# Performance work log

Measured on AMD Instinct MI355X. Metric: run time of the kernel, lower is better.

Reference implementation:

```python
import jax, jax.numpy as jnp
import numpy as np

B, H, W, C, N, P = 4, 200, 176, 256, 16384, 65536
EPS = 1e-3  # BatchNorm eps from the torch module


def _bn(x, g, b, axes):
    # training-mode batch norm (batch statistics), matching nn.BatchNorm forward
    m = x.mean(axes, keepdims=True)
    v = x.var(axes, keepdims=True)
    return (x - m) * jax.lax.rsqrt(v + EPS) * g + b


def setup_inputs() -> dict:
    key = jax.random.key(0)
    ks = jax.random.split(key, 16)
    s = 0.05
    d = {}
    d['feats'] = jax.random.normal(ks[0], (B, C, N), jnp.float32)
    d['cb'] = jax.random.randint(ks[1], (P,), 0, B, dtype=jnp.int32)
    d['cy'] = jax.random.randint(ks[2], (P,), 0, H, dtype=jnp.int32)
    d['cx'] = jax.random.randint(ks[3], (P,), 0, W, dtype=jnp.int32)
    # SH head: Linear(256,256,nb)+BN+ReLU, Linear(256,256,nb)+BN+ReLU, Linear(256,9,b)
    d['sh_w1'] = jax.random.normal(ks[4], (C, 256), jnp.float32) * s
    d['sh_g1'] = jnp.ones((256,), jnp.float32); d['sh_b1'] = jnp.zeros((256,), jnp.float32)
    d['sh_w2'] = jax.random.normal(ks[5], (256, 256), jnp.float32) * s
    d['sh_g2'] = jnp.ones((256,), jnp.float32); d['sh_b2'] = jnp.zeros((256,), jnp.float32)
    d['sh_w3'] = jax.random.normal(ks[6], (256, 9), jnp.float32) * s
    d['sh_bias3'] = jnp.zeros((9,), jnp.float32)
    # Gaus head: Linear(256,256,nb)+BN+ReLU, Linear(256,128,nb)+BN+ReLU, Linear(128,1,b)+sigmoid
    d['g_w1'] = jax.random.normal(ks[7], (C, 256), jnp.float32) * s
    d['g_g1'] = jnp.ones((256,), jnp.float32); d['g_b1'] = jnp.zeros((256,), jnp.float32)
    d['g_w2'] = jax.random.normal(ks[8], (256, 128), jnp.float32) * s
    d['g_g2'] = jnp.ones((128,), jnp.float32); d['g_b2'] = jnp.zeros((128,), jnp.float32)
    d['g_w3'] = jax.random.normal(ks[9], (128, 1), jnp.float32) * s
    d['g_bias3'] = jnp.zeros((1,), jnp.float32)
    # conv_out: 3x3 SparseConv2d no-bias + BN + ReLU ; shared_conv: 3x3 SubMConv2d bias + BN + ReLU
    d['cw1'] = jax.random.normal(ks[10], (3, 3, C, C), jnp.float32) * s
    d['c1_g'] = jnp.ones((C,), jnp.float32); d['c1_b'] = jnp.zeros((C,), jnp.float32)
    d['cw2'] = jax.random.normal(ks[11], (3, 3, C, C), jnp.float32) * s
    d['c2_bias'] = jnp.zeros((C,), jnp.float32)
    d['c2_g'] = jnp.ones((C,), jnp.float32); d['c2_b'] = jnp.zeros((C,), jnp.float32)
    return d


def reference(feats, cb, cy, cx, sh_w1, sh_g1, sh_b1, sh_w2, sh_g2, sh_b2, sh_w3, sh_bias3,
              g_w1, g_g1, g_b1, g_w2, g_g2, g_b2, g_w3, g_bias3,
              cw1, c1_g, c1_b, cw2, c2_bias, c2_g, c2_b):
    # [B,C,N] -> [B*N, C] point-wise features
    pw = feats.transpose(0, 2, 1).reshape(-1, C)
    # pool_feature_in_same_voxel: mean of point features sharing a voxel
    vid = cb * (H * W) + cy * W + cx  # [P] linear voxel id over dense BEV grid
    S = B * H * W
    sums = jax.ops.segment_sum(pw, vid, num_segments=S)            # [S, C]
    cnt = jax.ops.segment_sum(jnp.ones((P,), pw.dtype), vid, num_segments=S)
    pooled = sums / jnp.maximum(cnt, 1.0)[:, None]                 # [S, C]
    # SH head
    h = jax.nn.relu(_bn(pooled @ sh_w1, sh_g1, sh_b1, 0))
    h = jax.nn.relu(_bn(h @ sh_w2, sh_g2, sh_b2, 0))
    pred_sh = h @ sh_w3 + sh_bias3                                 # [S, 9]
    # Gaussian head
    g = jax.nn.relu(_bn(pooled @ g_w1, g_g1, g_b1, 0))
    g = jax.nn.relu(_bn(g @ g_w2, g_g2, g_b2, 0))
    pred_gaus = jax.nn.sigmoid(g @ g_w3 + g_bias3)                 # [S, 1]
    # get_sparse_voxel_feature3: SH (DC term) + gaussian modulated voxel features
    sp = pooled * pred_gaus * pred_sh[:, :1]                       # [S, C]
    x = sp.reshape(B, H, W, C)                                      # dense BEV sparse-tensor equivalent
    dn = ('NHWC', 'HWIO', 'NHWC')
    x = jax.lax.conv_general_dilated(x, cw1, (1, 1), 'SAME', dimension_numbers=dn)
    x = jax.nn.relu(_bn(x, c1_g, c1_b, (0, 1, 2)))
    x = jax.lax.conv_general_dilated(x, cw2, (1, 1), 'SAME', dimension_numbers=dn) + c2_bias
    x = jax.nn.relu(_bn(x, c2_g, c2_b, (0, 1, 2)))
    return x
```

## Files before the change

kernel.cpp:

```cpp
#include <hip/hip_runtime.h>
#include <hip/hip_bf16.h>
#include <cstdint>
#include <cstddef>

#define B_DIM 4
#define H_DIM 200
#define W_DIM 176
#define CCH 256
#define NPP 16384
#define NPTS 65536
#define HW 35200
#define S_TOT 140800
#define EPS 1e-3f
#define INV_S (1.0f/140800.0f)

typedef unsigned short ushort_t;
typedef __attribute__((ext_vector_type(8))) short bf16x8;
typedef __attribute__((ext_vector_type(4))) float f32x4;

__device__ __forceinline__ ushort_t f2bf(float f) {
    __hip_bfloat16 h = __float2bfloat16(f);
    return *(ushort_t*)&h;
}
__device__ __forceinline__ float bf2f(ushort_t u) {
    __hip_bfloat16 h = *(__hip_bfloat16*)&u;
    return __bfloat162float(h);
}

__device__ __forceinline__ void async16(const void* g, void* l) {
    __builtin_amdgcn_global_load_lds(
        (const __attribute__((address_space(1))) unsigned int*)g,
        (__attribute__((address_space(3))) unsigned int*)l,
        16, 0, 0);
}

__device__ __forceinline__ int xcd_virt(int fid, int n) {
    int q = n >> 3, r = n & 7;
    int xcd = fid & 7, idx = fid >> 3;
    int base = (xcd < r) ? xcd * (q + 1) : r * (q + 1) + (xcd - r) * q;
    return base + idx;
}

__global__ __launch_bounds__(256) void k_transpose(
    const float* __restrict__ feats, float* __restrict__ FT)
{
    __shared__ float lds[64][65];
    const int b  = blockIdx.z;
    const int c0 = blockIdx.y * 64;
    const int n0 = blockIdx.x * 64;
    const int tid = threadIdx.x;
#pragma unroll
    for (int i = 0; i < 16; ++i) {
        int idx = i * 256 + tid;
        int cr = idx >> 6, nc = idx & 63;
        lds[cr][nc] = feats[((size_t)b * 256 + c0 + cr) * NPP + n0 + nc];
    }
    __syncthreads();
#pragma unroll
    for (int i = 0; i < 16; ++i) {
        int idx = i * 256 + tid;
        int nr = idx >> 6, cc = idx & 63;
        FT[((size_t)b * NPP + n0 + nr) * CCH + c0 + cc] = lds[cc][nr];
    }
}

__global__ __launch_bounds__(256) void k_buildidx(
    const int* __restrict__ cb, const int* __restrict__ cy,
    const int* __restrict__ cx, int* __restrict__ cnt,
    int* __restrict__ pslot, int* __restrict__ vid)
{
    int p = blockIdx.x * 256 + threadIdx.x;
    int v = cb[p] * HW + cy[p] * W_DIM + cx[p];
    vid[p] = v;
    int r = atomicAdd(&cnt[v], 1);
    if (r < 8) pslot[v * 8 + r] = p;
}

__global__ __launch_bounds__(256) void k_poolgather(
    const float* __restrict__ FT, const int* __restrict__ cnt,
    const int* __restrict__ pslot, const int* __restrict__ vid,
    ushort_t* __restrict__ Pb)
{
    const int wave = threadIdx.x >> 6;
    const int lane = threadIdx.x & 63;
    const int v = blockIdx.x * 4 + wave;
    const int c = cnt[v];
    float4 a = make_float4(0.f, 0.f, 0.f, 0.f);
    if (c <= 8) {
        for (int k = 0; k < c; ++k) {
            int p = pslot[v * 8 + k];
            float4 r = ((const float4*)(FT + (size_t)p * CCH))[lane];
            a.x += r.x; a.y += r.y; a.z += r.z; a.w += r.w;
        }
    } else {
        for (int p = 0; p < NPTS; ++p)
            if (vid[p] == v) {
                float4 r = ((const float4*)(FT + (size_t)p * CCH))[lane];
                a.x += r.x; a.y += r.y; a.z += r.z; a.w += r.w;
            }
    }
    float inv = c ? 1.f / (float)c : 0.f;
    ushort4 o;
    o.x = f2bf(a.x * inv); o.y = f2bf(a.y * inv);
    o.z = f2bf(a.z * inv); o.w = f2bf(a.w * inv);
    ((ushort4*)(Pb + (size_t)v * CCH))[lane] = o;
}

__global__ __launch_bounds__(256) void k_gemmma(
    const ushort_t* __restrict__ X, const ushort_t* __restrict__ Wt,
    ushort_t* __restrict__ Y1, ushort_t* __restrict__ Y2, int ldY,
    int bnh, int nblocks,
    float* __restrict__ acc0, float* __restrict__ acc1, int sqoff)
{
    __shared__ ushort_t Asm[128 * 64];
    __shared__ ushort_t Bsm[128 * 64];
    const int tid  = threadIdx.x;
    const int w    = tid >> 6;
    const int lane = tid & 63;
    const int virt = xcd_virt(blockIdx.x, nblocks);
    const int pi   = virt / bnh;
    const int bn   = (virt % bnh) * 128;
    const int bm   = pi * 128;
    const int wr   = (w >> 1) * 64;
    const int wc   = (w & 1) * 64;

    size_t aoff[4]; size_t boff[4];
#pragma unroll
    for (int j = 0; j < 4; ++j) {
        int row  = 32 * j + 8 * w + (lane >> 3);
        int qlog = (lane & 7) ^ (row & 7);
        aoff[j] = (size_t)(bm + row) * 256 + qlog * 8;
        boff[j] = (size_t)(bn + row) * 256 + qlog * 8;
    }

    f32x4 acc[4][4] = {};
    for (int kc = 0; kc < 256; kc += 64) {
#pragma unroll
        for (int j = 0; j < 4; ++j)
            async16(X + aoff[j] + kc, Asm + (j * 32 + w * 8) * 64);
#pragma unroll
        for (int j = 0; j < 4; ++j)
            async16(Wt + boff[j] + kc, Bsm + (j * 32 + w * 8) * 64);
        __syncthreads();
#pragma unroll
        for (int ks = 0; ks < 2; ++ks) {
            const int q = ks * 4 + (lane >> 4);
            bf16x8 af[4], bfr[4];
#pragma unroll
            for (int i = 0; i < 4; ++i) {
                int ra = wr + i * 16 + (lane & 15);
                af[i] = *(const bf16x8*)&Asm[ra * 64 + ((q ^ (ra & 7)) * 8)];
            }
#pragma unroll
            for (int jn = 0; jn < 4; ++jn) {
                int rn = wc + jn * 16 + (lane & 15);
                bfr[jn] = *(const bf16x8*)&Bsm[rn * 64 + ((q ^ (rn & 7)) * 8)];
            }
#pragma unroll
            for (int i = 0; i < 4; ++i)
#pragma unroll
                for (int jn = 0; jn < 4; ++jn)
                    acc[i][jn] = __builtin_amdgcn_mfma_f32_16x16x32_bf16(
                        af[i], bfr[jn], acc[i][jn], 0, 0, 0);
        }
        __syncthreads();
    }

    const int crow0 = bm + wr + (lane >> 4) * 4;
    const int ccol0 = bn + wc + (lane & 15);
    float ls[4] = {}, lq[4] = {};
#pragma unroll
    for (int i = 0; i < 4; ++i)
#pragma unroll
        for (int jn = 0; jn < 4; ++jn) {
            int col = ccol0 + jn * 16;
#pragma unroll
            for (int r = 0; r < 4; ++r) {
                float v = acc[i][jn][r];
                ls[jn] += v; lq[jn] += v * v;
                size_t row = (size_t)(crow0 + i * 16 + r);
                if (col < 256) Y1[row * ldY + col] = f2bf(v);
                else           Y2[row * ldY + col - 256] = f2bf(v);
            }
        }
#pragma unroll
    for (int jn = 0; jn < 4; ++jn) {
        ls[jn] += __shfl_xor(ls[jn], 16, 64); ls[jn] += __shfl_xor(ls[jn], 32, 64);
        lq[jn] += __shfl_xor(lq[jn], 16, 64); lq[jn] += __shfl_xor(lq[jn], 32, 64);
    }
    float* red = (float*)Asm;
    if (lane < 16) {
#pragma unroll
        for (int jn = 0; jn < 4; ++jn) {
            red[((w * 16 + lane) * 4 + jn) * 2 + 0] = ls[jn];
            red[((w * 16 + lane) * 4 + jn) * 2 + 1] = lq[jn];
        }
    }
    __syncthreads();
    if (tid < 256) {
        int colhalf = tid & 127, isq = tid >> 7;
        int pair = colhalf >> 6, within = colhalf & 63;
        int l16 = within & 15, jn = within >> 4;
        int w0 = pair ? 1 : 0, w1 = pair ? 3 : 2;
        float s = red[((w0 * 16 + l16) * 4 + jn) * 2 + isq]
                + red[((w1 * 16 + l16) * 4 + jn) * 2 + isq];
        int colg = bn + colhalf;
        float* t = (colg < 256) ? acc0 : acc1;
        atomicAdd(&t[(colg & 255) + isq * sqoff], s);
    }
}

__global__ __launch_bounds__(256) void k_convmma(
    const ushort_t* __restrict__ X, const ushort_t* __restrict__ Wt,
    float* __restrict__ Yf, ushort_t* __restrict__ Yb,
    const float* __restrict__ bias, const ushort_t* __restrict__ zp,
    float* __restrict__ accp)
{
    __shared__ ushort_t Asm[2][192 * 64];
    __shared__ ushort_t Bsm[2][128 * 64];
    const int tid  = threadIdx.x;
    const int w    = tid >> 6;
    const int lane = tid & 63;
    const int virt = xcd_virt(blockIdx.x, 2200);
    const int pi   = virt >> 1;
    const int bn   = (virt & 1) * 128;
    const int b    = pi / 275;
    const int rem  = pi % 275;
    const int th   = rem / 11, tw = rem % 11;
    const int y0   = th * 8 - 1, x0 = tw * 16 - 1;
    const int hb   = (w >> 1) * 4;
    const int wc   = (w & 1) * 64;

    const int qlog = (lane & 7) ^ (lane >> 3);
    const ushort_t* asrc[6];
#pragma unroll
    for (int j = 0; j < 6; ++j) {
        int hr = j * 32 + w * 8 + (lane >> 3);
        int ph = hr / 18, pw = hr % 18;
        int y = y0 + ph, x = x0 + pw;
        bool ok = (hr < 180) && ((unsigned)y < (unsigned)H_DIM) &&
                  ((unsigned)x < (unsigned)W_DIM);
        asrc[j] = ok ? X + ((size_t)b * HW + (size_t)y * W_DIM + x) * 256 + qlog * 8
                     : zp + (lane & 7) * 8;
    }
    const ushort_t* bsrc = Wt + (size_t)(bn + w * 8 + (lane >> 3)) * 256 + qlog * 8;
    const int ldsoff = (w * 8) * 64;

#pragma unroll
    for (int j = 0; j < 6; ++j)
        async16(asrc[j], &Asm[0][(j * 32) * 64 + ldsoff]);
#pragma unroll
    for (int j = 0; j < 4; ++j)
        async16(bsrc + (size_t)j * 8192, &Bsm[0][(j * 32) * 64 + ldsoff]);
    __syncthreads();

    f32x4 acc[4][4] = {};
    for (int kc = 0; kc < 4; ++kc) {
        const ushort_t* acur = Asm[kc & 1];
#pragma unroll
        for (int pos = 0; pos < 9; ++pos) {
            const ushort_t* bcur = Bsm[(kc + pos) & 1];
            ushort_t* bnxt = (ushort_t*)Bsm[(kc + pos + 1) & 1];
            if (pos < 8) {
#pragma unroll
                for (int j = 0; j < 4; ++j)
                    async16(bsrc + (size_t)(pos + 1) * 65536 + kc * 64 + j * 8192,
                            bnxt + (j * 32) * 64 + ldsoff);
            } else if (kc < 3) {
#pragma unroll
                for (int j = 0; j < 4; ++j)
                    async16(bsrc + (size_t)(kc + 1) * 64 + j * 8192,
                            bnxt + (j * 32) * 64 + ldsoff);
#pragma unroll
                for (int j = 0; j < 6; ++j)
                    async16(asrc[j] + (kc + 1) * 64,
                            &Asm[(kc + 1) & 1][(j * 32) * 64 + ldsoff]);
            }
            const int dy = pos / 3 - 1, dx = pos % 3 - 1;
#pragma unroll
            for (int ks = 0; ks < 2; ++ks) {
                const int q = ks * 4 + (lane >> 4);
                bf16x8 af[4], bfr[4];
#pragma unroll
                for (int i = 0; i < 4; ++i) {
                    int ri = (hb + i + 1 + dy) * 18 + 1 + dx + (lane & 15);
                    af[i] = *(const bf16x8*)&acur[ri * 64 + ((q ^ (ri & 7)) * 8)];
                }
#pragma unroll
                for (int jn = 0; jn < 4; ++jn) {
                    int rn = wc + jn * 16 + (lane & 15);
                    bfr[jn] = *(const bf16x8*)&bcur[rn * 64 + ((q ^ (rn & 7)) * 8)];
                }
#pragma unroll
                for (int i = 0; i < 4; ++i)
#pragma unroll
                    for (int jn = 0; jn < 4; ++jn)
                        acc[i][jn] = __builtin_amdgcn_mfma_f32_16x16x32_bf16(
                            af[i], bfr[jn], acc[i][jn], 0, 0, 0);
            }
            __syncthreads();
        }
    }

    const size_t sbase = (size_t)b * HW + (size_t)(th * 8) * W_DIM + tw * 16;
    const int colb = bn + wc + (lane & 15);
    const int wsub = (lane >> 4) * 4;
    float ls[4] = {}, lq[4] = {};
#pragma unroll
    for (int i = 0; i < 4; ++i) {
        int h = hb + i;
#pragma unroll
        for (int jn = 0; jn < 4; ++jn) {
            int col = colb + jn * 16;
            float bb = bias ? bias[col] : 0.f;
#pragma unroll
            for (int r = 0; r < 4; ++r) {
                size_t s = sbase + (size_t)h * W_DIM + wsub + r;
                float v = acc[i][jn][r] + bb;
                ls[jn] += v; lq[jn] += v * v;
                size_t o = s * 256 + col;
                if (Yb) Yb[o] = f2bf(v); else Yf[o] = v;
            }
        }
    }
#pragma unroll
    for (int jn = 0; jn < 4; ++jn) {
        ls[jn] += __shfl_xor(ls[jn], 16, 64); ls[jn] += __shfl_xor(ls[jn], 32, 64);
        lq[jn] += __shfl_xor(lq[jn], 16, 64); lq[jn] += __shfl_xor(lq[jn], 32, 64);
    }
    float* red = (float*)&Asm[0][0];
    if (lane < 16) {
#pragma unroll
        for (int jn = 0; jn < 4; ++jn) {
            red[((w * 16 + lane) * 4 + jn) * 2 + 0] = ls[jn];
            red[((w * 16 + lane) * 4 + jn) * 2 + 1] = lq[jn];
        }
    }
    __syncthreads();
    if (tid < 256) {
        int colhalf = tid & 127, isq = tid >> 7;
        int pair = colhalf >> 6, within = colhalf & 63;
        int l16 = within & 15, jn = within >> 4;
        int w0 = pair ? 1 : 0, w1 = pair ? 3 : 2;
        float s = red[((w0 * 16 + l16) * 4 + jn) * 2 + isq]
                + red[((w1 * 16 + l16) * 4 + jn) * 2 + isq];
        atomicAdd(&accp[(bn + colhalf) + isq * 256], s);
    }
}

__global__ __launch_bounds__(256) void k_castw(
    const float* __restrict__ Wc, ushort_t* __restrict__ Wt, int CO)
{
    int pc = blockIdx.x;
    int co = pc % CO, pos = pc / CO, ci = threadIdx.x;
    Wt[(size_t)pc * 256 + ci] = f2bf(Wc[((size_t)pos * 256 + ci) * CO + co]);
}

__global__ void k_bnparams(const float* __restrict__ acc,
                           const float* __restrict__ g,
                           const float* __restrict__ b,
                           float* __restrict__ par, int ncols)
{
    int c = threadIdx.x;
    if (c >= ncols) return;
    float m = acc[c] * INV_S;
    float v = acc[ncols + c] * INV_S - m * m;
    float sc = g[c] * rsqrtf(v + EPS);
    par[c] = sc;
    par[ncols + c] = b[c] - m * sc;
}

__global__ __launch_bounds__(256) void k_bnrelu_bf(
    ushort_t* __restrict__ Y, const float* __restrict__ par)
{
    size_t q = (size_t)blockIdx.x * 256 + threadIdx.x;
    int c = (int)(q & 63) * 4;
    ushort4 u = ((ushort4*)Y)[q];
    u.x = f2bf(fmaxf(0.f, bf2f(u.x) * par[c + 0] + par[256 + c + 0]));
    u.y = f2bf(fmaxf(0.f, bf2f(u.y) * par[c + 1] + par[256 + c + 1]));
    u.z = f2bf(fmaxf(0.f, bf2f(u.z) * par[c + 2] + par[256 + c + 2]));
    u.w = f2bf(fmaxf(0.f, bf2f(u.w) * par[c + 3] + par[256 + c + 3]));
    ((ushort4*)Y)[q] = u;
}

__global__ __launch_bounds__(256) void k_headfin(
    const ushort_t* __restrict__ B2, const ushort_t* __restrict__ B3,
    const float* __restrict__ par1, const float* __restrict__ par3,
    const float* __restrict__ shw3, const float* __restrict__ shb3,
    const float* __restrict__ gw3, const float* __restrict__ gb3,
    const ushort_t* __restrict__ Pb, ushort_t* __restrict__ Xb)
{
    const int wave = threadIdx.x >> 6;
    const int lane = threadIdx.x & 63;
    const int s = blockIdx.x * 4 + wave;
    const ushort_t* b2 = B2 + (size_t)s * 256;
    const ushort_t* b3 = B3 + (size_t)s * 128;
    float d1 = 0.f, d2 = 0.f;
    {
        ushort4 u = ((const ushort4*)b2)[lane];
        int c = lane * 4;
        float v0 = fmaxf(0.f, bf2f(u.x) * par1[c + 0] + par1[256 + c + 0]);
        float v1 = fmaxf(0.f, bf2f(u.y) * par1[c + 1] + par1[256 + c + 1]);
        float v2 = fmaxf(0.f, bf2f(u.z) * par1[c + 2] + par1[256 + c + 2]);
        float v3 = fmaxf(0.f, bf2f(u.w) * par1[c + 3] + par1[256 + c + 3]);
        d1 = v0 * shw3[(c + 0) * 9] + v1 * shw3[(c + 1) * 9]
           + v2 * shw3[(c + 2) * 9] + v3 * shw3[(c + 3) * 9];
    }
    {
        ushort2 u = ((const ushort2*)b3)[lane];
        int c = lane * 2;
        float v0 = fmaxf(0.f, bf2f(u.x) * par3[c + 0] + par3[128 + c + 0]);
        float v1 = fmaxf(0.f, bf2f(u.y) * par3[c + 1] + par3[128 + c + 1]);
        d2 = v0 * gw3[c + 0] + v1 * gw3[c + 1];
    }
#pragma unroll
    for (int off = 32; off > 0; off >>= 1) {
        d1 += __shfl_down(d1, off, 64);
        d2 += __shfl_down(d2, off, 64);
    }
    d1 = __shfl(d1, 0, 64);
    d2 = __shfl(d2, 0, 64);
    float shdc = d1 + shb3[0];
    float gaus = 1.f / (1.f + expf(-(d2 + gb3[0])));
    float factor = shdc * gaus;
    ushort4 pv = ((const ushort4*)(Pb + (size_t)s * 256))[lane];
    ushort4 o;
    o.x = f2bf(bf2f(pv.x) * factor);
    o.y = f2bf(bf2f(pv.y) * factor);
    o.z = f2bf(bf2f(pv.z) * factor);
    o.w = f2bf(bf2f(pv.w) * factor);
    ((ushort4*)(Xb + (size_t)s * 256))[lane] = o;
}

__global__ __launch_bounds__(256) void k_bnrelu_inplace(
    float* __restrict__ Y, const float* __restrict__ par)
{
    size_t q = (size_t)blockIdx.x * 256 + threadIdx.x;
    int c = (int)(q & 63) * 4;
    float4* p = (float4*)Y;
    float4 v = p[q];
    v.x = fmaxf(0.f, v.x * par[c + 0] + par[256 + c + 0]);
    v.y = fmaxf(0.f, v.y * par[c + 1] + par[256 + c + 1]);
    v.z = fmaxf(0.f, v.z * par[c + 2] + par[256 + c + 2]);
    v.w = fmaxf(0.f, v.w * par[c + 3] + par[256 + c + 3]);
    p[q] = v;
}

extern "C" void kernel_launch(void* const* d_in, const int* in_sizes, int n_in,
                              void* d_out, int out_size, void* d_ws, size_t ws_size,
                              hipStream_t stream)
{
    (void)in_sizes; (void)n_in; (void)out_size; (void)ws_size;
    const float* feats   = (const float*)d_in[0];
    const int*   cb      = (const int*)d_in[1];
    const int*   cy      = (const int*)d_in[2];
    const int*   cx      = (const int*)d_in[3];
    const float* sh_w1   = (const float*)d_in[4];
    const float* sh_g1   = (const float*)d_in[5];
    const float* sh_b1   = (const float*)d_in[6];
    const float* sh_w2   = (const float*)d_in[7];
    const float* sh_g2   = (const float*)d_in[8];
    const float* sh_b2   = (const float*)d_in[9];
    const float* sh_w3   = (const float*)d_in[10];
    const float* sh_bias3= (const float*)d_in[11];
    const float* g_w1    = (const float*)d_in[12];
    const float* g_g1    = (const float*)d_in[13];
    const float* g_b1    = (const float*)d_in[14];
    const float* g_w2    = (const float*)d_in[15];
    const float* g_g2    = (const float*)d_in[16];
    const float* g_b2    = (const float*)d_in[17];
    const float* g_w3    = (const float*)d_in[18];
    const float* g_bias3 = (const float*)d_in[19];
    const float* cw1     = (const float*)d_in[20];
    const float* c1_g    = (const float*)d_in[21];
    const float* c1_b    = (const float*)d_in[22];
    const float* cw2     = (const float*)d_in[23];
    const float* c2_bias = (const float*)d_in[24];
    const float* c2_g    = (const float*)d_in[25];
    const float* c2_b    = (const float*)d_in[26];

    float* out = (float*)d_out;
    float* ws  = (float*)d_ws;
    ushort_t* Pb   = (ushort_t*)(ws);
    ushort_t* Bsh  = (ushort_t*)(ws + 18022400);
    ushort_t* Bg   = (ushort_t*)(ws + 36044800);
    ushort_t* Cb   = (ushort_t*)(ws + 54067200);
    float*    FT   = (float*)(ws + 54067200);
    ushort_t* Db   = (ushort_t*)(ws + 72089600);
    int*      CNTi = (int*)(ws + 72089600);
    int*      PSL  = CNTi + S_TOT;
    int*      VID  = PSL + S_TOT * 8;
    ushort_t* Eb   = Pb;
    ushort_t* WCAT = (ushort_t*)(ws + 81100800);
    ushort_t* WS2  = WCAT + 131072;
    ushort_t* WG2  = WS2 + 65536;
    ushort_t* WT1  = WG2 + 32768;
    ushort_t* WT2  = WT1 + 589824;
    ushort_t* ZP   = WT2 + 589824;
    float*    ACC  = (float*)(ZP + 2048);
    float*    PAR  = ACC + 6 * 512;

    hipMemsetAsync(CNTi, 0, (size_t)S_TOT * 4, stream);
    hipMemsetAsync(ACC, 0, 6 * 512 * 4, stream);
    hipMemsetAsync(ZP, 0, 4096, stream);

    k_castw<<<256, 256, 0, stream>>>(sh_w1, WCAT, 256);
    k_castw<<<256, 256, 0, stream>>>(g_w1, WCAT + 65536, 256);
    k_castw<<<256, 256, 0, stream>>>(sh_w2, WS2, 256);
    k_castw<<<128, 256, 0, stream>>>(g_w2, WG2, 128);
    k_castw<<<9 * 256, 256, 0, stream>>>(cw1, WT1, 256);
    k_castw<<<9 * 256, 256, 0, stream>>>(cw2, WT2, 256);

    k_transpose<<<dim3(256, 4, 4), 256, 0, stream>>>(feats, FT);
    k_buildidx<<<NPTS / 256, 256, 0, stream>>>(cb, cy, cx, CNTi, PSL, VID);
    k_poolgather<<<S_TOT / 4, 256, 0, stream>>>(FT, CNTi, PSL, VID, Pb);

    k_gemmma<<<4400, 256, 0, stream>>>(Pb, WCAT, Bsh, Bg, 256, 4, 4400,
                                       ACC + 0 * 512, ACC + 2 * 512, 256);
    k_bnparams<<<1, 256, 0, stream>>>(ACC + 0 * 512, sh_g1, sh_b1, PAR + 0 * 512, 256);
    k_bnparams<<<1, 256, 0, stream>>>(ACC + 2 * 512, g_g1, g_b1, PAR + 2 * 512, 256);
    k_bnrelu_bf<<<35200, 256, 0, stream>>>(Bsh, PAR + 0 * 512);
    k_bnrelu_bf<<<35200, 256, 0, stream>>>(Bg, PAR + 2 * 512);
    k_gemmma<<<2200, 256, 0, stream>>>(Bsh, WS2, Cb, Cb, 256, 2, 2200,
                                       ACC + 1 * 512, ACC + 1 * 512, 256);
    k_bnparams<<<1, 256, 0, stream>>>(ACC + 1 * 512, sh_g2, sh_b2, PAR + 1 * 512, 256);
    k_gemmma<<<1100, 256, 0, stream>>>(Bg, WG2, Db, Db, 128, 1, 1100,
                                       ACC + 3 * 512, ACC + 3 * 512, 128);
    k_bnparams<<<1, 128, 0, stream>>>(ACC + 3 * 512, g_g2, g_b2, PAR + 3 * 512, 128);
    k_headfin<<<S_TOT / 4, 256, 0, stream>>>(Cb, Db, PAR + 1 * 512, PAR + 3 * 512,
                                             sh_w3, sh_bias3, g_w3, g_bias3, Pb, Bsh);
    k_convmma<<<2200, 256, 0, stream>>>(Bsh, WT1, nullptr, Eb, nullptr, ZP,
                                        ACC + 4 * 512);
    k_bnparams<<<1, 256, 0, stream>>>(ACC + 4 * 512, c1_g, c1_b, PAR + 4 * 512, 256);
    k_bnrelu_bf<<<35200, 256, 0, stream>>>(Eb, PAR + 4 * 512);
    k_convmma<<<2200, 256, 0, stream>>>(Eb, WT2, out, nullptr, c2_bias, ZP,
                                        ACC + 5 * 512);
    k_bnparams<<<1, 256, 0, stream>>>(ACC + 5 * 512, c2_g, c2_b, PAR + 5 * 512, 256);
    k_bnrelu_inplace<<<35200, 256, 0, stream>>>(out, PAR + 5 * 512);
}
```

Baseline: 865.3 us.

## Double-buffer GEMM loads, fine-grained vmcnt waits, and bf16 intermediates for transpose/conv

The linear-head GEMM now double-buffers its LDS tiles with async global-to-LDS loads, prefetching the next K chunk while the current one computes. The conv kernel swaps __syncthreads for explicit vmcnt waits plus raw barriers, and both kernels raise wave priority around the MFMA loops. Separately, the transposed features are stored in bf16 instead of fp32. The second conv writes bf16 to scratch and the final BN+ReLU converts to fp32 output, cutting memory traffic at the cost of extra rounding in intermediates.

After: 811.6 us. 1.07x faster.

```diff
diff --git a/kernel.cpp b/kernel.cpp
--- a/kernel.cpp
+++ b/kernel.cpp
@@ -34,6 +34,12 @@
         16, 0, 0);
 }
 
+__device__ __forceinline__ void wait_vmcnt0()  { asm volatile("s_waitcnt vmcnt(0)" ::: "memory"); }
+__device__ __forceinline__ void wait_vmcnt4()  { asm volatile("s_waitcnt vmcnt(4)" ::: "memory"); }
+__device__ __forceinline__ void wait_vmcnt8()  { asm volatile("s_waitcnt vmcnt(8)" ::: "memory"); }
+__device__ __forceinline__ void wait_vmcnt10() { asm volatile("s_waitcnt vmcnt(10)" ::: "memory"); }
+__device__ __forceinline__ void memfence_compiler() { asm volatile("" ::: "memory"); }
+
 __device__ __forceinline__ int xcd_virt(int fid, int n) {
     int q = n >> 3, r = n & 7;
     int xcd = fid & 7, idx = fid >> 3;
@@ -42,7 +48,7 @@
 }
 
 __global__ __launch_bounds__(256) void k_transpose(
-    const float* __restrict__ feats, float* __restrict__ FT)
+    const float* __restrict__ feats, ushort_t* __restrict__ FT)
 {
     __shared__ float lds[64][65];
     const int b  = blockIdx.z;
@@ -60,7 +66,7 @@
     for (int i = 0; i < 16; ++i) {
         int idx = i * 256 + tid;
         int nr = idx >> 6, cc = idx & 63;
-        FT[((size_t)b * NPP + n0 + nr) * CCH + c0 + cc] = lds[cc][nr];
+        FT[((size_t)b * NPP + n0 + nr) * CCH + c0 + cc] = f2bf(lds[cc][nr]);
     }
 }
 
@@ -77,7 +83,7 @@
 }
 
 __global__ __launch_bounds__(256) void k_poolgather(
-    const float* __restrict__ FT, const int* __restrict__ cnt,
+    const ushort_t* __restrict__ FT, const int* __restrict__ cnt,
     const int* __restrict__ pslot, const int* __restrict__ vid,
     ushort_t* __restrict__ Pb)
 {
@@ -85,24 +91,24 @@
     const int lane = threadIdx.x & 63;
     const int v = blockIdx.x * 4 + wave;
     const int c = cnt[v];
-    float4 a = make_float4(0.f, 0.f, 0.f, 0.f);
+    float a0 = 0.f, a1 = 0.f, a2 = 0.f, a3 = 0.f;
     if (c <= 8) {
         for (int k = 0; k < c; ++k) {
             int p = pslot[v * 8 + k];
-            float4 r = ((const float4*)(FT + (size_t)p * CCH))[lane];
-            a.x += r.x; a.y += r.y; a.z += r.z; a.w += r.w;
+            ushort4 r = ((const ushort4*)(FT + (size_t)p * CCH))[lane];
+            a0 += bf2f(r.x); a1 += bf2f(r.y); a2 += bf2f(r.z); a3 += bf2f(r.w);
         }
     } else {
         for (int p = 0; p < NPTS; ++p)
             if (vid[p] == v) {
-                float4 r = ((const float4*)(FT + (size_t)p * CCH))[lane];
-                a.x += r.x; a.y += r.y; a.z += r.z; a.w += r.w;
+                ushort4 r = ((const ushort4*)(FT + (size_t)p * CCH))[lane];
+                a0 += bf2f(r.x); a1 += bf2f(r.y); a2 += bf2f(r.z); a3 += bf2f(r.w);
             }
     }
     float inv = c ? 1.f / (float)c : 0.f;
     ushort4 o;
-    o.x = f2bf(a.x * inv); o.y = f2bf(a.y * inv);
-    o.z = f2bf(a.z * inv); o.w = f2bf(a.w * inv);
+    o.x = f2bf(a0 * inv); o.y = f2bf(a1 * inv);
+    o.z = f2bf(a2 * inv); o.w = f2bf(a3 * inv);
     ((ushort4*)(Pb + (size_t)v * CCH))[lane] = o;
 }
 
@@ -112,8 +118,8 @@
     int bnh, int nblocks,
     float* __restrict__ acc0, float* __restrict__ acc1, int sqoff)
 {
-    __shared__ ushort_t Asm[128 * 64];
-    __shared__ ushort_t Bsm[128 * 64];
+    __shared__ ushort_t Asm[2][128 * 64];
+    __shared__ ushort_t Bsm[2][128 * 64];
     const int tid  = threadIdx.x;
     const int w    = tid >> 6;
     const int lane = tid & 63;
@@ -132,16 +138,30 @@
         aoff[j] = (size_t)(bm + row) * 256 + qlog * 8;
         boff[j] = (size_t)(bn + row) * 256 + qlog * 8;
     }
+    const int lo = (w * 8) * 64;
+
+#pragma unroll
+    for (int j = 0; j < 4; ++j) async16(X + aoff[j], &Asm[0][(j * 32) * 64 + lo]);
+#pragma unroll
+    for (int j = 0; j < 4; ++j) async16(Wt + boff[j], &Bsm[0][(j * 32) * 64 + lo]);
 
     f32x4 acc[4][4] = {};
-    for (int kc = 0; kc < 256; kc += 64) {
-#pragma unroll
-        for (int j = 0; j < 4; ++j)
-            async16(X + aoff[j] + kc, Asm + (j * 32 + w * 8) * 64);
-#pragma unroll
-        for (int j = 0; j < 4; ++j)
-            async16(Wt + boff[j] + kc, Bsm + (j * 32 + w * 8) * 64);
-        __syncthreads();
+    for (int kc = 0; kc < 4; ++kc) {
+        if (kc < 3) {
+#pragma unroll
+            for (int j = 0; j < 4; ++j)
+                async16(X + aoff[j] + (kc + 1) * 64, &Asm[(kc + 1) & 1][(j * 32) * 64 + lo]);
+#pragma unroll
+            for (int j = 0; j < 4; ++j)
+                async16(Wt + boff[j] + (kc + 1) * 64, &Bsm[(kc + 1) & 1][(j * 32) * 64 + lo]);
+            wait_vmcnt8();
+        } else {
+            wait_vmcnt0();
+        }
+        __builtin_amdgcn_s_barrier();
+        const ushort_t* Ac = Asm[kc & 1];
+        const ushort_t* Bc = Bsm[kc & 1];
+        __builtin_amdgcn_s_setprio(1);
 #pragma unroll
         for (int ks = 0; ks < 2; ++ks) {
             const int q = ks * 4 + (lane >> 4);
@@ -149,12 +169,12 @@
 #pragma unroll
             for (int i = 0; i < 4; ++i) {
                 int ra = wr + i * 16 + (lane & 15);
-                af[i] = *(const bf16x8*)&Asm[ra * 64 + ((q ^ (ra & 7)) * 8)];
+                af[i] = *(const bf16x8*)&Ac[ra * 64 + ((q ^ (ra & 7)) * 8)];
             }
 #pragma unroll
             for (int jn = 0; jn < 4; ++jn) {
                 int rn = wc + jn * 16 + (lane & 15);
-                bfr[jn] = *(const bf16x8*)&Bsm[rn * 64 + ((q ^ (rn & 7)) * 8)];
+                bfr[jn] = *(const bf16x8*)&Bc[rn * 64 + ((q ^ (rn & 7)) * 8)];
             }
 #pragma unroll
             for (int i = 0; i < 4; ++i)
@@ -163,8 +183,11 @@
                     acc[i][jn] = __builtin_amdgcn_mfma_f32_16x16x32_bf16(
                         af[i], bfr[jn], acc[i][jn], 0, 0, 0);
         }
-        __syncthreads();
-    }
+        __builtin_amdgcn_s_setprio(0);
+        memfence_compiler();
+        __builtin_amdgcn_s_barrier();
+    }
+    __syncthreads();
 
     const int crow0 = bm + wr + (lane >> 4) * 4;
     const int ccol0 = bn + wc + (lane & 15);
@@ -188,7 +211,7 @@
         ls[jn] += __shfl_xor(ls[jn], 16, 64); ls[jn] += __shfl_xor(ls[jn], 32, 64);
         lq[jn] += __shfl_xor(lq[jn], 16, 64); lq[jn] += __shfl_xor(lq[jn], 32, 64);
     }
-    float* red = (float*)Asm;
+    float* red = (float*)&Asm[0][0];
     if (lane < 16) {
 #pragma unroll
         for (int jn = 0; jn < 4; ++jn) {
@@ -212,9 +235,8 @@
 
 __global__ __launch_bounds__(256) void k_convmma(
     const ushort_t* __restrict__ X, const ushort_t* __restrict__ Wt,
-    float* __restrict__ Yf, ushort_t* __restrict__ Yb,
-    const float* __restrict__ bias, const ushort_t* __restrict__ zp,
-    float* __restrict__ accp)
+    ushort_t* __restrict__ Yb, const float* __restrict__ bias,
+    const ushort_t* __restrict__ zp, float* __restrict__ accp)
 {
     __shared__ ushort_t Asm[2][192 * 64];
     __shared__ ushort_t Bsm[2][128 * 64];
@@ -244,15 +266,14 @@
                      : zp + (lane & 7) * 8;
     }
     const ushort_t* bsrc = Wt + (size_t)(bn + w * 8 + (lane >> 3)) * 256 + qlog * 8;
-    const int ldsoff = (w * 8) * 64;
+    const int lo = (w * 8) * 64;
 
 #pragma unroll
     for (int j = 0; j < 6; ++j)
-        async16(asrc[j], &Asm[0][(j * 32) * 64 + ldsoff]);
+        async16(asrc[j], &Asm[0][(j * 32) * 64 + lo]);
 #pragma unroll
     for (int j = 0; j < 4; ++j)
-        async16(bsrc + (size_t)j * 8192, &Bsm[0][(j * 32) * 64 + ldsoff]);
-    __syncthreads();
+        async16(bsrc + (size_t)j * 8192, &Bsm[0][(j * 32) * 64 + lo]);
 
     f32x4 acc[4][4] = {};
     for (int kc = 0; kc < 4; ++kc) {
@@ -261,22 +282,42 @@
         for (int pos = 0; pos < 9; ++pos) {
             const ushort_t* bcur = Bsm[(kc + pos) & 1];
             ushort_t* bnxt = (ushort_t*)Bsm[(kc + pos + 1) & 1];
-            if (pos < 8) {
+            if (pos == 0) {
+                if (kc < 3) {
+#pragma unroll
+                    for (int j = 0; j < 6; ++j)
+                        async16(asrc[j] + (kc + 1) * 64,
+                                &Asm[(kc + 1) & 1][(j * 32) * 64 + lo]);
+#pragma unroll
+                    for (int j = 0; j < 4; ++j)
+                        async16(bsrc + (size_t)65536 + kc * 64 + j * 8192,
+                                bnxt + (j * 32) * 64 + lo);
+                    wait_vmcnt10();
+                } else {
+#pragma unroll
+                    for (int j = 0; j < 4; ++j)
+                        async16(bsrc + (size_t)65536 + kc * 64 + j * 8192,
+                                bnxt + (j * 32) * 64 + lo);
+                    wait_vmcnt4();
+                }
+            } else if (pos < 8) {
 #pragma unroll
                 for (int j = 0; j < 4; ++j)
                     async16(bsrc + (size_t)(pos + 1) * 65536 + kc * 64 + j * 8192,
-                            bnxt + (j * 32) * 64 + ldsoff);
+                            bnxt + (j * 32) * 64 + lo);
+                wait_vmcnt4();
             } else if (kc < 3) {
 #pragma unroll
                 for (int j = 0; j < 4; ++j)
                     async16(bsrc + (size_t)(kc + 1) * 64 + j * 8192,
-                            bnxt + (j * 32) * 64 + ldsoff);
-#pragma unroll
-                for (int j = 0; j < 6; ++j)
-                    async16(asrc[j] + (kc + 1) * 64,
-                            &Asm[(kc + 1) & 1][(j * 32) * 64 + ldsoff]);
-            }
+                            bnxt + (j * 32) * 64 + lo);
+                wait_vmcnt4();
+            } else {
+                wait_vmcnt0();
+            }
+            __builtin_amdgcn_s_barrier();
             const int dy = pos / 3 - 1, dx = pos % 3 - 1;
+            __builtin_amdgcn_s_setprio(1);
 #pragma unroll
             for (int ks = 0; ks < 2; ++ks) {
                 const int q = ks * 4 + (lane >> 4);
@@ -298,9 +339,12 @@
                         acc[i][jn] = __builtin_amdgcn_mfma_f32_16x16x32_bf16(
                             af[i], bfr[jn], acc[i][jn], 0, 0, 0);
             }
-            __syncthreads();
-        }
-    }
+            __builtin_amdgcn_s_setprio(0);
+            memfence_compiler();
+            __builtin_amdgcn_s_barrier();
+        }
+    }
+    __syncthreads();
 
     const size_t sbase = (size_t)b * HW + (size_t)(th * 8) * W_DIM + tw * 16;
     const int colb = bn + wc + (lane & 15);
@@ -318,8 +362,7 @@
                 size_t s = sbase + (size_t)h * W_DIM + wsub + r;
                 float v = acc[i][jn][r] + bb;
                 ls[jn] += v; lq[jn] += v * v;
-                size_t o = s * 256 + col;
-                if (Yb) Yb[o] = f2bf(v); else Yf[o] = v;
+                Yb[s * 256 + col] = f2bf(v);
             }
         }
     }
@@ -432,18 +475,19 @@
     ((ushort4*)(Xb + (size_t)s * 256))[lane] = o;
 }
 
-__global__ __launch_bounds__(256) void k_bnrelu_inplace(
-    float* __restrict__ Y, const float* __restrict__ par)
+__global__ __launch_bounds__(256) void k_bnrelu_f32out(
+    const ushort_t* __restrict__ Y, const float* __restrict__ par,
+    float* __restrict__ out)
 {
     size_t q = (size_t)blockIdx.x * 256 + threadIdx.x;
     int c = (int)(q & 63) * 4;
-    float4* p = (float4*)Y;
-    float4 v = p[q];
-    v.x = fmaxf(0.f, v.x * par[c + 0] + par[256 + c + 0]);
-    v.y = fmaxf(0.f, v.y * par[c + 1] + par[256 + c + 1]);
-    v.z = fmaxf(0.f, v.z * par[c + 2] + par[256 + c + 2]);
-    v.w = fmaxf(0.f, v.w * par[c + 3] + par[256 + c + 3]);
-    p[q] = v;
+    ushort4 u = ((const ushort4*)Y)[q];
+    float4 v;
+    v.x = fmaxf(0.f, bf2f(u.x) * par[c + 0] + par[256 + c + 0]);
+    v.y = fmaxf(0.f, bf2f(u.y) * par[c + 1] + par[256 + c + 1]);
+    v.z = fmaxf(0.f, bf2f(u.z) * par[c + 2] + par[256 + c + 2]);
+    v.w = fmaxf(0.f, bf2f(u.w) * par[c + 3] + par[256 + c + 3]);
+    ((float4*)out)[q] = v;
 }
 
 extern "C" void kernel_launch(void* const* d_in, const int* in_sizes, int n_in,
@@ -485,7 +529,7 @@
     ushort_t* Bsh  = (ushort_t*)(ws + 18022400);
     ushort_t* Bg   = (ushort_t*)(ws + 36044800);
     ushort_t* Cb   = (ushort_t*)(ws + 54067200);
-    float*    FT   = (float*)(ws + 54067200);
+    ushort_t* FT   = (ushort_t*)(ws + 54067200);
     ushort_t* Db   = (ushort_t*)(ws + 72089600);
     int*      CNTi = (int*)(ws + 72089600);
     int*      PSL  = CNTi + S_TOT;
@@ -529,12 +573,10 @@
     k_bnparams<<<1, 128, 0, stream>>>(ACC + 3 * 512, g_g2, g_b2, PAR + 3 * 512, 128);
     k_headfin<<<S_TOT / 4, 256, 0, stream>>>(Cb, Db, PAR + 1 * 512, PAR + 3 * 512,
                                              sh_w3, sh_bias3, g_w3, g_bias3, Pb, Bsh);
-    k_convmma<<<2200, 256, 0, stream>>>(Bsh, WT1, nullptr, Eb, nullptr, ZP,
-                                        ACC + 4 * 512);
+    k_convmma<<<2200, 256, 0, stream>>>(Bsh, WT1, Eb, nullptr, ZP, ACC + 4 * 512);
     k_bnparams<<<1, 256, 0, stream>>>(ACC + 4 * 512, c1_g, c1_b, PAR + 4 * 512, 256);
     k_bnrelu_bf<<<35200, 256, 0, stream>>>(Eb, PAR + 4 * 512);
-    k_convmma<<<2200, 256, 0, stream>>>(Eb, WT2, out, nullptr, c2_bias, ZP,
-                                        ACC + 5 * 512);
+    k_convmma<<<2200, 256, 0, stream>>>(Eb, WT2, Bsh, c2_bias, ZP, ACC + 5 * 512);
     k_bnparams<<<1, 256, 0, stream>>>(ACC + 5 * 512, c2_g, c2_b, PAR + 5 * 512, 256);
-    k_bnrelu_inplace<<<35200, 256, 0, stream>>>(out, PAR + 5 * 512);
-}
+    k_bnrelu_f32out<<<35200, 256, 0, stream>>>(Bsh, PAR + 5 * 512, out);
+}
```
